# Optimization experiments

Hardware: AMD Instinct MI355X
Metric: run time of the kernel (lower is better)

The kernel has to match this reference:

```python
import jax, jax.numpy as jnp
import numpy as np

B, N, D = 8, 256, 256
LN_EPS = 1e-5


def setup_inputs() -> dict:
    key = jax.random.key(0)
    ks = jax.random.split(key, 8)
    s1 = 1.0 / np.sqrt(2 * D)  # torch Linear init scale ~ U(-1/sqrt(fan_in), ...); use normal*scale
    s2 = 1.0 / np.sqrt(D)
    return {
        "patch_features": jax.random.normal(ks[0], (B, N, D), dtype=jnp.float32),
        # relation_transform: Linear(2D, D) -> ReLU -> Linear(D, 1)
        "W1": jax.random.normal(ks[1], (2 * D, D), dtype=jnp.float32) * s1,
        "b1": jax.random.normal(ks[2], (D,), dtype=jnp.float32) * s1,
        "W2": jax.random.normal(ks[3], (D, 1), dtype=jnp.float32) * s2,
        "b2": jax.random.normal(ks[4], (1,), dtype=jnp.float32) * s2,
        # context_projection: Linear(D, D) + LayerNorm(D)
        "Wp": jax.random.normal(ks[5], (D, D), dtype=jnp.float32) * s2,
        "bp": jax.random.normal(ks[6], (D,), dtype=jnp.float32) * s2,
        "ln_gamma": jnp.ones((D,), dtype=jnp.float32),
        "ln_beta": jnp.zeros((D,), dtype=jnp.float32),
    }


def reference(patch_features, W1, b1, W2, b2, Wp, bp, ln_gamma, ln_beta):
    x = patch_features  # [B, N, D]
    d = x.shape[-1]
    # cat([x_i, x_j]) @ W1 == x_i @ W1[:D] + x_j @ W1[D:]
    hi = jnp.einsum("bnd,de->bne", x, W1[:d])   # [B, N, D]
    hj = jnp.einsum("bmd,de->bme", x, W1[d:])   # [B, N, D]
    h = jax.nn.relu(hi[:, :, None, :] + hj[:, None, :, :] + b1)  # [B, N, N, D]
    scores = jnp.einsum("bnmd,do->bnm", h, W2) + b2[0]            # [B, N, N]
    # diagonal entries stay exactly 0 (original never fills i == j)
    eye = jnp.eye(scores.shape[1], dtype=bool)
    scores = jnp.where(eye[None, :, :], 0.0, scores)
    weights = jax.nn.softmax(scores, axis=2)                      # [B, N, N]
    ctx = jnp.einsum("bnm,bmd->bnd", weights, x)                  # [B, N, D]
    proj = jnp.einsum("bnd,de->bne", ctx, Wp) + bp
    mu = jnp.mean(proj, axis=-1, keepdims=True)
    var = jnp.mean(jnp.square(proj - mu), axis=-1, keepdims=True)
    ln = (proj - mu) * jax.lax.rsqrt(var + LN_EPS) * ln_gamma + ln_beta
    return x + ln
```

## Files before the change

kernel.cpp:

```cpp
#include <hip/hip_runtime.h>

#define LN_EPS 1e-5f

__device__ __forceinline__ float wred_max(float v) {
#pragma unroll
    for (int off = 32; off; off >>= 1) v = fmaxf(v, __shfl_xor(v, off, 64));
    return v;
}
__device__ __forceinline__ float wred_sum(float v) {
#pragma unroll
    for (int off = 32; off; off >>= 1) v += __shfl_xor(v, off, 64);
    return v;
}

__global__ __launch_bounds__(256) void k_gemm_hij(
    const float* __restrict__ x,
    const float* __restrict__ W1,
    const float* __restrict__ b1,
    float* __restrict__ hi_ws,
    float* __restrict__ hjT)
{
    __shared__ __align__(16) float xs[4][256];
    const int t = threadIdx.x;
    const int row0 = blockIdx.x * 4;

    ((float4*)&xs[0][0])[t] = ((const float4*)(x + (size_t)row0 * 256))[t];
    __syncthreads();

    const int half = t >> 7;
    const int e2 = (t & 127) * 2;
    const float* Wb = W1 + (size_t)half * 65536 + e2;

    float a0[4], a1[4];
#pragma unroll
    for (int r = 0; r < 4; r++) { a0[r] = 0.f; a1[r] = 0.f; }

    for (int k = 0; k < 256; k += 4) {
        float2 w0 = *(const float2*)(Wb + (size_t)(k + 0) * 256);
        float2 w1 = *(const float2*)(Wb + (size_t)(k + 1) * 256);
        float2 w2 = *(const float2*)(Wb + (size_t)(k + 2) * 256);
        float2 w3 = *(const float2*)(Wb + (size_t)(k + 3) * 256);
#pragma unroll
        for (int r = 0; r < 4; r++) {
            float4 xr = *(const float4*)&xs[r][k];
            a0[r] = fmaf(xr.x, w0.x, a0[r]); a1[r] = fmaf(xr.x, w0.y, a1[r]);
            a0[r] = fmaf(xr.y, w1.x, a0[r]); a1[r] = fmaf(xr.y, w1.y, a1[r]);
            a0[r] = fmaf(xr.z, w2.x, a0[r]); a1[r] = fmaf(xr.z, w2.y, a1[r]);
            a0[r] = fmaf(xr.w, w3.x, a0[r]); a1[r] = fmaf(xr.w, w3.y, a1[r]);
        }
    }

    if (half == 0) {
        float add0 = b1[e2], add1 = b1[e2 + 1];
#pragma unroll
        for (int r = 0; r < 4; r++)
            *(float2*)&hi_ws[(size_t)(row0 + r) * 256 + e2] =
                make_float2(a0[r] + add0, a1[r] + add1);
    } else {
        const int b = row0 >> 8, mloc = row0 & 255;
        *(float4*)&hjT[((size_t)(b * 256 + e2)) * 256 + mloc] =
            make_float4(a0[0], a0[1], a0[2], a0[3]);
        *(float4*)&hjT[((size_t)(b * 256 + e2 + 1)) * 256 + mloc] =
            make_float4(a1[0], a1[1], a1[2], a1[3]);
    }
}

__global__ __launch_bounds__(256) void k_fused(
    const float* __restrict__ x,
    const float* __restrict__ hi_ws,
    const float* __restrict__ hjT,
    const float* __restrict__ W2, const float* __restrict__ b2,
    const float* __restrict__ Wp, const float* __restrict__ bp,
    const float* __restrict__ gma, const float* __restrict__ bta,
    float* __restrict__ out)
{
    const int t = threadIdx.x;
    const int lane = t & 63, wv = t >> 6;
    const int bn0 = blockIdx.x * 4;
    const int b = bn0 >> 8, n0 = bn0 & 255;

    __shared__ __align__(16) float hi_s[4][256];
    __shared__ __align__(16) float w2_s[256];
    __shared__ __align__(16) float wt_s[4][256];
    __shared__ __align__(16) float ctx_s[4][256];
    __shared__ float part[8][4];

#pragma unroll
    for (int i = 0; i < 4; i++) hi_s[i][t] = hi_ws[(size_t)(bn0 + i) * 256 + t];
    w2_s[t] = W2[t];
    __syncthreads();

    const float* hjb = hjT + (size_t)b * 65536 + t;
    float s[4] = {0.f, 0.f, 0.f, 0.f};
    for (int d = 0; d < 256; d += 4) {
        float h0 = hjb[(size_t)(d + 0) * 256];
        float h1 = hjb[(size_t)(d + 1) * 256];
        float h2 = hjb[(size_t)(d + 2) * 256];
        float h3 = hjb[(size_t)(d + 3) * 256];
        float4 w4 = *(const float4*)&w2_s[d];
#pragma unroll
        for (int i = 0; i < 4; i++) {
            float4 hi4 = *(const float4*)&hi_s[i][d];
            s[i] = fmaf(fmaxf(hi4.x + h0, 0.f), w4.x, s[i]);
            s[i] = fmaf(fmaxf(hi4.y + h1, 0.f), w4.y, s[i]);
            s[i] = fmaf(fmaxf(hi4.z + h2, 0.f), w4.z, s[i]);
            s[i] = fmaf(fmaxf(hi4.w + h3, 0.f), w4.w, s[i]);
        }
    }
    float b2v = b2[0];
#pragma unroll
    for (int i = 0; i < 4; i++) {
        s[i] += b2v;
        if (t == n0 + i) s[i] = 0.f;
    }

#pragma unroll
    for (int i = 0; i < 4; i++) {
        float m = wred_max(s[i]);
        if (lane == 0) part[i][wv] = m;
    }
    __syncthreads();
    float ev[4];
#pragma unroll
    for (int i = 0; i < 4; i++) {
        float mx = fmaxf(fmaxf(part[i][0], part[i][1]),
                         fmaxf(part[i][2], part[i][3]));
        ev[i] = __expf(s[i] - mx);
        float sm = wred_sum(ev[i]);
        if (lane == 0) part[4 + i][wv] = sm;
    }
    __syncthreads();
#pragma unroll
    for (int i = 0; i < 4; i++) {
        float tot = (part[4 + i][0] + part[4 + i][1]) +
                    (part[4 + i][2] + part[4 + i][3]);
        wt_s[i][t] = ev[i] / tot;
    }
    __syncthreads();

    const float* xb = x + (size_t)b * 65536 + t;
    float c[4] = {0.f, 0.f, 0.f, 0.f};
    for (int m = 0; m < 256; m += 4) {
        float x0 = xb[(size_t)(m + 0) * 256];
        float x1 = xb[(size_t)(m + 1) * 256];
        float x2 = xb[(size_t)(m + 2) * 256];
        float x3 = xb[(size_t)(m + 3) * 256];
#pragma unroll
        for (int i = 0; i < 4; i++) {
            float4 w4 = *(const float4*)&wt_s[i][m];
            c[i] = fmaf(w4.x, x0, c[i]);
            c[i] = fmaf(w4.y, x1, c[i]);
            c[i] = fmaf(w4.z, x2, c[i]);
            c[i] = fmaf(w4.w, x3, c[i]);
        }
    }
#pragma unroll
    for (int i = 0; i < 4; i++) ctx_s[i][t] = c[i];
    __syncthreads();

    float bpv = bp[t];
    float p[4] = {bpv, bpv, bpv, bpv};
    const float* Wc = Wp + t;
    for (int d = 0; d < 256; d += 4) {
        float q0 = Wc[(size_t)(d + 0) * 256];
        float q1 = Wc[(size_t)(d + 1) * 256];
        float q2 = Wc[(size_t)(d + 2) * 256];
        float q3 = Wc[(size_t)(d + 3) * 256];
#pragma unroll
        for (int i = 0; i < 4; i++) {
            float4 c4 = *(const float4*)&ctx_s[i][d];
            p[i] = fmaf(c4.x, q0, p[i]);
            p[i] = fmaf(c4.y, q1, p[i]);
            p[i] = fmaf(c4.z, q2, p[i]);
            p[i] = fmaf(c4.w, q3, p[i]);
        }
    }

#pragma unroll
    for (int i = 0; i < 4; i++) {
        float su = wred_sum(p[i]);
        float sq = wred_sum(p[i] * p[i]);
        if (lane == 0) { part[i][wv] = su; part[4 + i][wv] = sq; }
    }
    __syncthreads();
    float gv = gma[t], bv = bta[t];
#pragma unroll
    for (int i = 0; i < 4; i++) {
        float su = (part[i][0] + part[i][1]) + (part[i][2] + part[i][3]);
        float sq = (part[4 + i][0] + part[4 + i][1]) +
                   (part[4 + i][2] + part[4 + i][3]);
        float mu = su * (1.f / 256.f);
        float var = sq * (1.f / 256.f) - mu * mu;
        float ln = (p[i] - mu) * rsqrtf(var + LN_EPS) * gv + bv;
        out[(size_t)(bn0 + i) * 256 + t] = x[(size_t)(bn0 + i) * 256 + t] + ln;
    }
}

extern "C" void kernel_launch(void* const* d_in, const int* in_sizes, int n_in,
                              void* d_out, int out_size, void* d_ws, size_t ws_size,
                              hipStream_t stream) {
    const float* x   = (const float*)d_in[0];
    const float* W1  = (const float*)d_in[1];
    const float* b1  = (const float*)d_in[2];
    const float* W2  = (const float*)d_in[3];
    const float* b2  = (const float*)d_in[4];
    const float* Wp  = (const float*)d_in[5];
    const float* bp  = (const float*)d_in[6];
    const float* gma = (const float*)d_in[7];
    const float* bta = (const float*)d_in[8];
    float* out = (float*)d_out;

    float* hi_ws = (float*)d_ws;
    float* hjT   = hi_ws + (size_t)2048 * 256;

    k_gemm_hij<<<512, 256, 0, stream>>>(x, W1, b1, hi_ws, hjT);
    k_fused<<<512, 256, 0, stream>>>(x, hi_ws, hjT, W2, b2, Wp, bp,
                                     gma, bta, out);
}
```

Before: 130.5 us.

## Use float4 loads and split-K across waves with shared-memory reduction

Both kernels now have each lane own four consecutive output columns, so global loads become float4 and fewer, wider memory instructions are issued. In the fused kernel, the score, context and projection reductions are split along K across the four waves (64 each). Partial results are combined through a new 16 KB shared buffer. The GEMM kernel splits rows across wave pairs instead of columns. This adds extra syncs and shared memory, which may lower occupancy, and the transposed hjT stores are now scattered scalar writes.

```diff
diff --git a/kernel.cpp b/kernel.cpp
--- a/kernel.cpp
+++ b/kernel.cpp
@@ -22,46 +22,59 @@
 {
     __shared__ __align__(16) float xs[4][256];
     const int t = threadIdx.x;
+    const int lane = t & 63, w = t >> 6;
     const int row0 = blockIdx.x * 4;
 
-    ((float4*)&xs[0][0])[t] = ((const float4*)(x + (size_t)row0 * 256))[t];
-    __syncthreads();
-
-    const int half = t >> 7;
-    const int e2 = (t & 127) * 2;
-    const float* Wb = W1 + (size_t)half * 65536 + e2;
-
-    float a0[4], a1[4];
-#pragma unroll
-    for (int r = 0; r < 4; r++) { a0[r] = 0.f; a1[r] = 0.f; }
-
+    ((float4*)xs)[t] = ((const float4*)(x + (size_t)row0 * 256))[t];
+    __syncthreads();
+
+    const int half = w >> 1;
+    const int r0 = (w & 1) * 2;
+    const float* Wb = W1 + (size_t)half * 65536 + 4 * lane;
+
+    float a00 = 0.f, a01 = 0.f, a02 = 0.f, a03 = 0.f;
+    float a10 = 0.f, a11 = 0.f, a12 = 0.f, a13 = 0.f;
+
+#pragma unroll 2
     for (int k = 0; k < 256; k += 4) {
-        float2 w0 = *(const float2*)(Wb + (size_t)(k + 0) * 256);
-        float2 w1 = *(const float2*)(Wb + (size_t)(k + 1) * 256);
-        float2 w2 = *(const float2*)(Wb + (size_t)(k + 2) * 256);
-        float2 w3 = *(const float2*)(Wb + (size_t)(k + 3) * 256);
-#pragma unroll
-        for (int r = 0; r < 4; r++) {
-            float4 xr = *(const float4*)&xs[r][k];
-            a0[r] = fmaf(xr.x, w0.x, a0[r]); a1[r] = fmaf(xr.x, w0.y, a1[r]);
-            a0[r] = fmaf(xr.y, w1.x, a0[r]); a1[r] = fmaf(xr.y, w1.y, a1[r]);
-            a0[r] = fmaf(xr.z, w2.x, a0[r]); a1[r] = fmaf(xr.z, w2.y, a1[r]);
-            a0[r] = fmaf(xr.w, w3.x, a0[r]); a1[r] = fmaf(xr.w, w3.y, a1[r]);
-        }
+        float4 q0 = *(const float4*)(Wb + (size_t)(k + 0) * 256);
+        float4 q1 = *(const float4*)(Wb + (size_t)(k + 1) * 256);
+        float4 q2 = *(const float4*)(Wb + (size_t)(k + 2) * 256);
+        float4 q3 = *(const float4*)(Wb + (size_t)(k + 3) * 256);
+        float4 xa = *(const float4*)&xs[r0][k];
+        float4 xb = *(const float4*)&xs[r0 + 1][k];
+        a00 = fmaf(xa.x, q0.x, a00); a00 = fmaf(xa.y, q1.x, a00);
+        a00 = fmaf(xa.z, q2.x, a00); a00 = fmaf(xa.w, q3.x, a00);
+        a01 = fmaf(xa.x, q0.y, a01); a01 = fmaf(xa.y, q1.y, a01);
+        a01 = fmaf(xa.z, q2.y, a01); a01 = fmaf(xa.w, q3.y, a01);
+        a02 = fmaf(xa.x, q0.z, a02); a02 = fmaf(xa.y, q1.z, a02);
+        a02 = fmaf(xa.z, q2.z, a02); a02 = fmaf(xa.w, q3.z, a02);
+        a03 = fmaf(xa.x, q0.w, a03); a03 = fmaf(xa.y, q1.w, a03);
+        a03 = fmaf(xa.z, q2.w, a03); a03 = fmaf(xa.w, q3.w, a03);
+        a10 = fmaf(xb.x, q0.x, a10); a10 = fmaf(xb.y, q1.x, a10);
+        a10 = fmaf(xb.z, q2.x, a10); a10 = fmaf(xb.w, q3.x, a10);
+        a11 = fmaf(xb.x, q0.y, a11); a11 = fmaf(xb.y, q1.y, a11);
+        a11 = fmaf(xb.z, q2.y, a11); a11 = fmaf(xb.w, q3.y, a11);
+        a12 = fmaf(xb.x, q0.z, a12); a12 = fmaf(xb.y, q1.z, a12);
+        a12 = fmaf(xb.z, q2.z, a12); a12 = fmaf(xb.w, q3.z, a12);
+        a13 = fmaf(xb.x, q0.w, a13); a13 = fmaf(xb.y, q1.w, a13);
+        a13 = fmaf(xb.z, q2.w, a13); a13 = fmaf(xb.w, q3.w, a13);
     }
 
     if (half == 0) {
-        float add0 = b1[e2], add1 = b1[e2 + 1];
-#pragma unroll
-        for (int r = 0; r < 4; r++)
-            *(float2*)&hi_ws[(size_t)(row0 + r) * 256 + e2] =
-                make_float2(a0[r] + add0, a1[r] + add1);
+        float4 b4 = *(const float4*)(b1 + 4 * lane);
+        float4 o0 = make_float4(a00 + b4.x, a01 + b4.y, a02 + b4.z, a03 + b4.w);
+        float4 o1 = make_float4(a10 + b4.x, a11 + b4.y, a12 + b4.z, a13 + b4.w);
+        *(float4*)&hi_ws[(size_t)(row0 + r0 + 0) * 256 + 4 * lane] = o0;
+        *(float4*)&hi_ws[(size_t)(row0 + r0 + 1) * 256 + 4 * lane] = o1;
     } else {
-        const int b = row0 >> 8, mloc = row0 & 255;
-        *(float4*)&hjT[((size_t)(b * 256 + e2)) * 256 + mloc] =
-            make_float4(a0[0], a0[1], a0[2], a0[3]);
-        *(float4*)&hjT[((size_t)(b * 256 + e2 + 1)) * 256 + mloc] =
-            make_float4(a1[0], a1[1], a1[2], a1[3]);
+        const int b = row0 >> 8;
+        const int m = (row0 & 255) + r0;
+        float* base = hjT + (size_t)b * 65536 + (size_t)(4 * lane) * 256 + m;
+        base[0 * 256 + 0] = a00; base[1 * 256 + 0] = a01;
+        base[2 * 256 + 0] = a02; base[3 * 256 + 0] = a03;
+        base[0 * 256 + 1] = a10; base[1 * 256 + 1] = a11;
+        base[2 * 256 + 1] = a12; base[3 * 256 + 1] = a13;
     }
 }
 
@@ -75,7 +88,7 @@
     float* __restrict__ out)
 {
     const int t = threadIdx.x;
-    const int lane = t & 63, wv = t >> 6;
+    const int lane = t & 63, w = t >> 6;
     const int bn0 = blockIdx.x * 4;
     const int b = bn0 >> 8, n0 = bn0 & 255;
 
@@ -83,6 +96,7 @@
     __shared__ __align__(16) float w2_s[256];
     __shared__ __align__(16) float wt_s[4][256];
     __shared__ __align__(16) float ctx_s[4][256];
+    __shared__ __align__(16) float sred[4][4][256];
     __shared__ float part[8][4];
 
 #pragma unroll
@@ -90,34 +104,61 @@
     w2_s[t] = W2[t];
     __syncthreads();
 
-    const float* hjb = hjT + (size_t)b * 65536 + t;
-    float s[4] = {0.f, 0.f, 0.f, 0.f};
-    for (int d = 0; d < 256; d += 4) {
-        float h0 = hjb[(size_t)(d + 0) * 256];
-        float h1 = hjb[(size_t)(d + 1) * 256];
-        float h2 = hjb[(size_t)(d + 2) * 256];
-        float h3 = hjb[(size_t)(d + 3) * 256];
-        float4 w4 = *(const float4*)&w2_s[d];
-#pragma unroll
-        for (int i = 0; i < 4; i++) {
-            float4 hi4 = *(const float4*)&hi_s[i][d];
-            s[i] = fmaf(fmaxf(hi4.x + h0, 0.f), w4.x, s[i]);
-            s[i] = fmaf(fmaxf(hi4.y + h1, 0.f), w4.y, s[i]);
-            s[i] = fmaf(fmaxf(hi4.z + h2, 0.f), w4.z, s[i]);
-            s[i] = fmaf(fmaxf(hi4.w + h3, 0.f), w4.w, s[i]);
+    {
+        const float* hjp = hjT + (size_t)b * 65536 + (size_t)(w * 64) * 256 + 4 * lane;
+        float sp[4][4];
+#pragma unroll
+        for (int n = 0; n < 4; n++)
+#pragma unroll
+            for (int j = 0; j < 4; j++) sp[n][j] = 0.f;
+
+#pragma unroll 2
+        for (int dc = 0; dc < 64; dc += 4) {
+            float4 h0 = *(const float4*)(hjp + (size_t)(dc + 0) * 256);
+            float4 h1 = *(const float4*)(hjp + (size_t)(dc + 1) * 256);
+            float4 h2 = *(const float4*)(hjp + (size_t)(dc + 2) * 256);
+            float4 h3 = *(const float4*)(hjp + (size_t)(dc + 3) * 256);
+            float4 wq = *(const float4*)&w2_s[w * 64 + dc];
+#pragma unroll
+            for (int n = 0; n < 4; n++) {
+                float4 hi4 = *(const float4*)&hi_s[n][w * 64 + dc];
+                sp[n][0] = fmaf(fmaxf(hi4.x + h0.x, 0.f), wq.x, sp[n][0]);
+                sp[n][0] = fmaf(fmaxf(hi4.y + h1.x, 0.f), wq.y, sp[n][0]);
+                sp[n][0] = fmaf(fmaxf(hi4.z + h2.x, 0.f), wq.z, sp[n][0]);
+                sp[n][0] = fmaf(fmaxf(hi4.w + h3.x, 0.f), wq.w, sp[n][0]);
+                sp[n][1] = fmaf(fmaxf(hi4.x + h0.y, 0.f), wq.x, sp[n][1]);
+                sp[n][1] = fmaf(fmaxf(hi4.y + h1.y, 0.f), wq.y, sp[n][1]);
+                sp[n][1] = fmaf(fmaxf(hi4.z + h2.y, 0.f), wq.z, sp[n][1]);
+                sp[n][1] = fmaf(fmaxf(hi4.w + h3.y, 0.f), wq.w, sp[n][1]);
+                sp[n][2] = fmaf(fmaxf(hi4.x + h0.z, 0.f), wq.x, sp[n][2]);
+                sp[n][2] = fmaf(fmaxf(hi4.y + h1.z, 0.f), wq.y, sp[n][2]);
+                sp[n][2] = fmaf(fmaxf(hi4.z + h2.z, 0.f), wq.z, sp[n][2]);
+                sp[n][2] = fmaf(fmaxf(hi4.w + h3.z, 0.f), wq.w, sp[n][2]);
+                sp[n][3] = fmaf(fmaxf(hi4.x + h0.w, 0.f), wq.x, sp[n][3]);
+                sp[n][3] = fmaf(fmaxf(hi4.y + h1.w, 0.f), wq.y, sp[n][3]);
+                sp[n][3] = fmaf(fmaxf(hi4.z + h2.w, 0.f), wq.z, sp[n][3]);
+                sp[n][3] = fmaf(fmaxf(hi4.w + h3.w, 0.f), wq.w, sp[n][3]);
+            }
         }
-    }
+#pragma unroll
+        for (int n = 0; n < 4; n++)
+            *(float4*)&sred[w][n][4 * lane] =
+                make_float4(sp[n][0], sp[n][1], sp[n][2], sp[n][3]);
+    }
+    __syncthreads();
+
     float b2v = b2[0];
-#pragma unroll
-    for (int i = 0; i < 4; i++) {
-        s[i] += b2v;
+    float s[4];
+#pragma unroll
+    for (int i = 0; i < 4; i++) {
+        s[i] = ((sred[0][i][t] + sred[1][i][t]) +
+                (sred[2][i][t] + sred[3][i][t])) + b2v;
         if (t == n0 + i) s[i] = 0.f;
     }
-
 #pragma unroll
     for (int i = 0; i < 4; i++) {
         float m = wred_max(s[i]);
-        if (lane == 0) part[i][wv] = m;
+        if (lane == 0) part[i][w] = m;
     }
     __syncthreads();
     float ev[4];
@@ -127,7 +168,7 @@
                          fmaxf(part[i][2], part[i][3]));
         ev[i] = __expf(s[i] - mx);
         float sm = wred_sum(ev[i]);
-        if (lane == 0) part[4 + i][wv] = sm;
+        if (lane == 0) part[4 + i][w] = sm;
     }
     __syncthreads();
 #pragma unroll
@@ -138,49 +179,107 @@
     }
     __syncthreads();
 
-    const float* xb = x + (size_t)b * 65536 + t;
-    float c[4] = {0.f, 0.f, 0.f, 0.f};
-    for (int m = 0; m < 256; m += 4) {
-        float x0 = xb[(size_t)(m + 0) * 256];
-        float x1 = xb[(size_t)(m + 1) * 256];
-        float x2 = xb[(size_t)(m + 2) * 256];
-        float x3 = xb[(size_t)(m + 3) * 256];
-#pragma unroll
-        for (int i = 0; i < 4; i++) {
-            float4 w4 = *(const float4*)&wt_s[i][m];
-            c[i] = fmaf(w4.x, x0, c[i]);
-            c[i] = fmaf(w4.y, x1, c[i]);
-            c[i] = fmaf(w4.z, x2, c[i]);
-            c[i] = fmaf(w4.w, x3, c[i]);
+    {
+        const float* xpp = x + (size_t)b * 65536 + (size_t)(w * 64) * 256 + 4 * lane;
+        float cp[4][4];
+#pragma unroll
+        for (int n = 0; n < 4; n++)
+#pragma unroll
+            for (int j = 0; j < 4; j++) cp[n][j] = 0.f;
+
+#pragma unroll 2
+        for (int mc = 0; mc < 64; mc += 4) {
+            float4 x0 = *(const float4*)(xpp + (size_t)(mc + 0) * 256);
+            float4 x1 = *(const float4*)(xpp + (size_t)(mc + 1) * 256);
+            float4 x2 = *(const float4*)(xpp + (size_t)(mc + 2) * 256);
+            float4 x3 = *(const float4*)(xpp + (size_t)(mc + 3) * 256);
+#pragma unroll
+            for (int n = 0; n < 4; n++) {
+                float4 wt4 = *(const float4*)&wt_s[n][w * 64 + mc];
+                cp[n][0] = fmaf(wt4.x, x0.x, cp[n][0]);
+                cp[n][0] = fmaf(wt4.y, x1.x, cp[n][0]);
+                cp[n][0] = fmaf(wt4.z, x2.x, cp[n][0]);
+                cp[n][0] = fmaf(wt4.w, x3.x, cp[n][0]);
+                cp[n][1] = fmaf(wt4.x, x0.y, cp[n][1]);
+                cp[n][1] = fmaf(wt4.y, x1.y, cp[n][1]);
+                cp[n][1] = fmaf(wt4.z, x2.y, cp[n][1]);
+                cp[n][1] = fmaf(wt4.w, x3.y, cp[n][1]);
+                cp[n][2] = fmaf(wt4.x, x0.z, cp[n][2]);
+                cp[n][2] = fmaf(wt4.y, x1.z, cp[n][2]);
+                cp[n][2] = fmaf(wt4.z, x2.z, cp[n][2]);
+                cp[n][2] = fmaf(wt4.w, x3.z, cp[n][2]);
+                cp[n][3] = fmaf(wt4.x, x0.w, cp[n][3]);
+                cp[n][3] = fmaf(wt4.y, x1.w, cp[n][3]);
+                cp[n][3] = fmaf(wt4.z, x2.w, cp[n][3]);
+                cp[n][3] = fmaf(wt4.w, x3.w, cp[n][3]);
+            }
         }
-    }
-#pragma unroll
-    for (int i = 0; i < 4; i++) ctx_s[i][t] = c[i];
+#pragma unroll
+        for (int n = 0; n < 4; n++)
+            *(float4*)&sred[w][n][4 * lane] =
+                make_float4(cp[n][0], cp[n][1], cp[n][2], cp[n][3]);
+    }
+    __syncthreads();
+#pragma unroll
+    for (int i = 0; i < 4; i++)
+        ctx_s[i][t] = (sred[0][i][t] + sred[1][i][t]) +
+                      (sred[2][i][t] + sred[3][i][t]);
+    __syncthreads();
+
+    {
+        const float* wpp = Wp + (size_t)(w * 64) * 256 + 4 * lane;
+        float pq[4][4];
+#pragma unroll
+        for (int n = 0; n < 4; n++)
+#pragma unroll
+            for (int j = 0; j < 4; j++) pq[n][j] = 0.f;
+
+#pragma unroll 2
+        for (int dc = 0; dc < 64; dc += 4) {
+            float4 q0 = *(const float4*)(wpp + (size_t)(dc + 0) * 256);
+            float4 q1 = *(const float4*)(wpp + (size_t)(dc + 1) * 256);
+            float4 q2 = *(const float4*)(wpp + (size_t)(dc + 2) * 256);
+            float4 q3 = *(const float4*)(wpp + (size_t)(dc + 3) * 256);
+#pragma unroll
+            for (int n = 0; n < 4; n++) {
+                float4 c4 = *(const float4*)&ctx_s[n][w * 64 + dc];
+                pq[n][0] = fmaf(c4.x, q0.x, pq[n][0]);
+                pq[n][0] = fmaf(c4.y, q1.x, pq[n][0]);
+                pq[n][0] = fmaf(c4.z, q2.x, pq[n][0]);
+                pq[n][0] = fmaf(c4.w, q3.x, pq[n][0]);
+                pq[n][1] = fmaf(c4.x, q0.y, pq[n][1]);
+                pq[n][1] = fmaf(c4.y, q1.y, pq[n][1]);
+                pq[n][1] = fmaf(c4.z, q2.y, pq[n][1]);
+                pq[n][1] = fmaf(c4.w, q3.y, pq[n][1]);
+                pq[n][2] = fmaf(c4.x, q0.z, pq[n][2]);
+                pq[n][2] = fmaf(c4.y, q1.z, pq[n][2]);
+                pq[n][2] = fmaf(c4.z, q2.z, pq[n][2]);
+                pq[n][2] = fmaf(c4.w, q3.z, pq[n][2]);
+                pq[n][3] = fmaf(c4.x, q0.w, pq[n][3]);
+                pq[n][3] = fmaf(c4.y, q1.w, pq[n][3]);
+                pq[n][3] = fmaf(c4.z, q2.w, pq[n][3]);
+                pq[n][3] = fmaf(c4.w, q3.w, pq[n][3]);
+            }
+        }
+#pragma unroll
+        for (int n = 0; n < 4; n++)
+            *(float4*)&sred[w][n][4 * lane] =
+                make_float4(pq[n][0], pq[n][1], pq[n][2], pq[n][3]);
+    }
     __syncthreads();
 
     float bpv = bp[t];
-    float p[4] = {bpv, bpv, bpv, bpv};
-    const float* Wc = Wp + t;
-    for (int d = 0; d < 256; d += 4) {
-        float q0 = Wc[(size_t)(d + 0) * 256];
-        float q1 = Wc[(size_t)(d + 1) * 256];
-        float q2 = Wc[(size_t)(d + 2) * 256];
-        float q3 = Wc[(size_t)(d + 3) * 256];
-#pragma unroll
-        for (int i = 0; i < 4; i++) {
-            float4 c4 = *(const float4*)&ctx_s[i][d];
-            p[i] = fmaf(c4.x, q0, p[i]);
-            p[i] = fmaf(c4.y, q1, p[i]);
-            p[i] = fmaf(c4.z, q2, p[i]);
-            p[i] = fmaf(c4.w, q3, p[i]);
-        }
-    }
+    float p[4];
+#pragma unroll
+    for (int i = 0; i < 4; i++)
+        p[i] = ((sred[0][i][t] + sred[1][i][t]) +
+                (sred[2][i][t] + sred[3][i][t])) + bpv;
 
 #pragma unroll
     for (int i = 0; i < 4; i++) {
         float su = wred_sum(p[i]);
         float sq = wred_sum(p[i] * p[i]);
-        if (lane == 0) { part[i][wv] = su; part[4 + i][wv] = sq; }
+        if (lane == 0) { part[i][w] = su; part[4 + i][w] = sq; }
     }
     __syncthreads();
     float gv = gma[t], bv = bta[t];
```

New measurement: 113.4 us. 1.15x faster.
